# Kernel tuning notes

Measured on AMD Instinct MI355X. Metric: run time of the kernel, lower is better.

The kernel has to match this reference:

```python
import jax, jax.numpy as jnp
import numpy as np


def setup_inputs() -> dict:
    key = jax.random.key(0)
    k1, k2, k3, k4 = jax.random.split(key, 4)
    bs, n, f_in, f_out, n_head = 8, 2048, 64, 32, 4
    return {
        "h": jax.random.normal(k1, (bs, n, f_in), dtype=jnp.float32),
        "w": jax.random.normal(k2, (n_head, f_in, f_out), dtype=jnp.float32) * 0.1,
        "a_src": jax.random.normal(k3, (n_head, f_out, 1), dtype=jnp.float32) * 0.1,
        "a_dst": jax.random.normal(k4, (n_head, f_out, 1), dtype=jnp.float32) * 0.1,
        "b": jnp.zeros((f_out,), dtype=jnp.float32),
    }


def reference(h, w, a_src, a_dst, b):
    # h: [bs, n, f_in], w: [H, f_in, f_out]
    # h_prime: [bs, H, n, f_out]
    h_prime = jnp.einsum("bnf,hfo->bhno", h, w)
    # additive scores: attn_src[b,h,i] + attn_dst[b,h,j]
    attn_src = jnp.einsum("bhno,ho->bhn", h_prime, a_src[..., 0])  # [bs,H,n]
    attn_dst = jnp.einsum("bhno,ho->bhn", h_prime, a_dst[..., 0])  # [bs,H,n]
    attn = attn_src[:, :, :, None] + attn_dst[:, :, None, :]       # [bs,H,n,n]
    attn = jax.nn.leaky_relu(attn, negative_slope=0.2)
    attn = jax.nn.softmax(attn, axis=-1)
    # dropout with p=0.0 (eval) is identity
    output = jnp.einsum("bhij,bhjo->bhio", attn, h_prime) + b
    return (output, attn)
```

## Files before the change

### kernel.cpp

```cpp
#include <hip/hip_runtime.h>
#include <hip/hip_bf16.h>

#define BS 8
#define NH 4
#define NSEQ 2048
#define FIN 64
#define FOUT 32
#define CH 32
#define BHH (BS*NH)
#define NBINS 8192
#define LOG2E 1.44269504088896340736f

typedef float f32x4 __attribute__((ext_vector_type(4)));

#define WSS_SE    0
#define WSS_DE    (WSS_SE + BHH*NSEQ)
#define WSS_INVL  (WSS_DE + BHH*NSEQ)
#define WSS_KEY   (WSS_INVL + BHH*NSEQ)
#define WSS_SUFL  (WSS_KEY + BHH*NSEQ)
#define WSS_PREL  (WSS_SUFL + BHH*NSEQ)
#define WSS_TOTP  (WSS_PREL + BHH*NSEQ)
#define WSS_TOTN  (WSS_TOTP + BHH*16)
#define WSS_VTOTP (WSS_TOTN + BHH*16)
#define WSS_VTOTN (WSS_VTOTP + BHH*16*CH)
#define WSS_FTOT  (WSS_VTOTN + BHH*16*CH)
#define WSI_SIDX  0

#define BIG_HP    0
#define BIG_SUFP  (BIG_HP + BHH*NSEQ*CH)
#define BIG_PREN  (BIG_SUFP + BHH*NSEQ*CH)
#define BIG_TOTAL (BIG_PREN + BHH*NSEQ*CH)

__global__ __launch_bounds__(256) void k1_proj(
    const float* __restrict__ h, const float* __restrict__ w,
    const float* __restrict__ asrc, const float* __restrict__ adst,
    float* __restrict__ ws, float* __restrict__ big)
{
    __shared__ float hl[64*65];
    const int b  = blockIdx.x >> 5;
    const int i0 = (blockIdx.x & 31) * 64;
    const int tid = threadIdx.x;
    const float* hsrc = h + ((size_t)b*NSEQ + i0)*FIN;
    for (int x = tid; x < 64*64; x += 256) hl[(x>>6)*65 + (x&63)] = hsrc[x];
    __syncthreads();
    const int head = __builtin_amdgcn_readfirstlane(tid >> 6);
    const int r = tid & 63;
    const int i = i0 + r;
    float acc[FOUT];
#pragma unroll
    for (int o=0;o<FOUT;o++) acc[o]=0.f;
    const float* wh = w + head*FIN*FOUT;
    for (int f=0; f<FIN; f++) {
        const float hv = hl[r*65+f];
#pragma unroll
        for (int o=0;o<FOUT;o++) acc[o] += hv * wh[f*FOUT+o];
    }
    const float* as = asrc + head*FOUT;
    const float* ad = adst + head*FOUT;
    float s=0.f, d=0.f;
#pragma unroll
    for (int o=0;o<FOUT;o++){ s += acc[o]*as[o]; d += acc[o]*ad[o]; }
    const int bh = b*NH + head;
    float* hp = big + BIG_HP + ((size_t)bh*NSEQ + i)*CH;
#pragma unroll
    for (int o=0;o<FOUT;o+=4) { f32x4 v = {acc[o],acc[o+1],acc[o+2],acc[o+3]}; *(f32x4*)(hp+o)=v; }
    ws[WSS_SE + bh*NSEQ + i] = s * LOG2E;
    ws[WSS_DE + bh*NSEQ + i] = d * LOG2E;
}

__global__ __launch_bounds__(1024) void kh_sort(
    float* __restrict__ ws, int* __restrict__ wsi)
{
    __shared__ int hist[NBINS];
    __shared__ int wtot[16];
    const int bh = blockIdx.x;
    const int tid = threadIdx.x;
    const int wv = tid >> 6, lane = tid & 63;
    const float x0 = ws[WSS_DE + bh*NSEQ + tid];
    const float x1 = ws[WSS_DE + bh*NSEQ + tid + 1024];
    for (int bb=tid; bb<NBINS; bb+=1024) hist[bb]=0;
    __syncthreads();
    int b0 = (int)((x0 + 8.0f)*512.0f); b0 = b0 > NBINS-1 ? NBINS-1 : (b0 < 0 ? 0 : b0);
    int b1 = (int)((x1 + 8.0f)*512.0f); b1 = b1 > NBINS-1 ? NBINS-1 : (b1 < 0 ? 0 : b1);
    atomicAdd(&hist[b0],1); atomicAdd(&hist[b1],1);
    __syncthreads();
    int loc[8]; int tsum=0;
#pragma unroll
    for (int k=0;k<8;k++){ loc[k]=tsum; tsum += hist[tid*8+k]; }
    int inc = tsum;
#pragma unroll
    for (int off=1; off<64; off<<=1){ int v=__shfl_up(inc,off); if (lane>=off) inc+=v; }
    if (lane==63) wtot[wv]=inc;
    const int laneex = inc - tsum;
    __syncthreads();
    if (tid==0){ int a=0; for (int k=0;k<16;k++){ int v=wtot[k]; wtot[k]=a; a+=v; } }
    __syncthreads();
    const int base = wtot[wv] + laneex;
#pragma unroll
    for (int k=0;k<8;k++) hist[tid*8+k] = base + loc[k];
    __syncthreads();
    {
        int p0 = atomicAdd(&hist[b0],1);
        ws[WSS_KEY + bh*NSEQ + p0] = x0; wsi[WSI_SIDX + bh*NSEQ + p0] = tid;
        int p1 = atomicAdd(&hist[b1],1);
        ws[WSS_KEY + bh*NSEQ + p1] = x1; wsi[WSI_SIDX + bh*NSEQ + p1] = tid + 1024;
    }
}

__global__ __launch_bounds__(256) void k2b(
    float* __restrict__ ws, const int* __restrict__ wsi, float* __restrict__ big)
{
    __shared__ float kk[128];
    __shared__ int   si[128];
    __shared__ float SP[128][CH];
    __shared__ float SN[128][CH];
    const int bid = blockIdx.x;
    const int bh = bid >> 4, c = bid & 15;
    const int tid = threadIdx.x, wv = tid>>6, lane = tid&63;
    if (tid < 128) {
        kk[tid] = ws[WSS_KEY + bh*NSEQ + c*128 + tid];
        si[tid] = wsi[WSI_SIDX + bh*NSEQ + c*128 + tid];
    }
    __syncthreads();
    const float* hpb = big + BIG_HP + (size_t)bh*NSEQ*CH;
    const int half = lane >> 5, ch = lane & 31;
#pragma unroll 4
    for (int t=0; t<16; t++) {
        const int rr = wv*32 + t*2 + half;
        const float dk = kk[rr];
        const float v  = hpb[(size_t)si[rr]*CH + ch];
        SP[rr][ch] = __builtin_amdgcn_exp2f(dk)      * v;
        SN[rr][ch] = __builtin_amdgcn_exp2f(0.2f*dk) * v;
    }
    __syncthreads();
    const size_t tb = (size_t)bh*NSEQ + c*128;
    if (wv == 0 && lane < CH) {
        float acc = 0.f;
        for (int rr=127; rr>=0; rr--) {
            acc += SP[rr][lane];
            big[BIG_SUFP + (tb + rr)*CH + lane] = acc;
        }
        ws[WSS_VTOTP + (bh*16 + c)*CH + lane] = acc;
    } else if (wv == 1 && lane < CH) {
        float acc = 0.f;
        for (int rr=0; rr<128; rr++) {
            big[BIG_PREN + (tb + rr)*CH + lane] = acc;
            acc += SN[rr][lane];
        }
        ws[WSS_VTOTN + (bh*16 + c)*CH + lane] = acc;
    } else if (wv == 2 && lane == 0) {
        float acc = 0.f;
        for (int rr=127; rr>=0; rr--) {
            acc += __builtin_amdgcn_exp2f(kk[rr]);
            ws[WSS_SUFL + tb + rr] = acc;
        }
        ws[WSS_TOTP + bh*16 + c] = acc;
    } else if (wv == 3 && lane == 0) {
        float acc = 0.f;
        for (int rr=0; rr<128; rr++) {
            ws[WSS_PREL + tb + rr] = acc;
            acc += __builtin_amdgcn_exp2f(0.2f*kk[rr]);
        }
        ws[WSS_TOTN + bh*16 + c] = acc;
    }
}

__global__ __launch_bounds__(256) void k2c(
    float* __restrict__ ws, const float* __restrict__ big,
    const float* __restrict__ bvec, float* __restrict__ outp)
{
    __shared__ float keys[NSEQ];
    __shared__ float sufl[NSEQ];
    __shared__ float prel[NSEQ];
    __shared__ float vofP[17][CH];
    __shared__ float vofN[17][CH];
    __shared__ float sofP[17], sofN[17];
    __shared__ int   krow[128];
    __shared__ float invrow[128], e1row[128], e2row[128];
    const int bid = blockIdx.x;
    const int bh = bid >> 4, q = bid & 15;
    const int tid = threadIdx.x, wv = tid>>6, lane = tid&63;
    for (int x = tid; x < NSEQ; x += 256) {
        keys[x] = ws[WSS_KEY  + bh*NSEQ + x];
        sufl[x] = ws[WSS_SUFL + bh*NSEQ + x];
        prel[x] = ws[WSS_PREL + bh*NSEQ + x];
    }
    if (tid < CH) {
        float a = 0.f;
        for (int c=15; c>=0; c--) { vofP[c][tid] = a; a += ws[WSS_VTOTP + (bh*16+c)*CH + tid]; }
        vofP[16][tid] = 0.f;
        a = 0.f;
        for (int c=0; c<16; c++) { vofN[c][tid] = a; a += ws[WSS_VTOTN + (bh*16+c)*CH + tid]; }
        vofN[16][tid] = a;
    } else if (tid == 64) {
        float a = 0.f;
        for (int c=15; c>=0; c--) { sofP[c] = a; a += ws[WSS_TOTP + bh*16 + c]; }
        sofP[16] = 0.f;
        a = 0.f;
        for (int c=0; c<16; c++) { sofN[c] = a; a += ws[WSS_TOTN + bh*16 + c]; }
        sofN[16] = a;
    }
    __syncthreads();
    if (tid < 128) {
        const int i = q*128 + tid;
        const float sp = ws[WSS_SE + bh*NSEQ + i];
        const float tau = -sp;
        int lo=0, hi=NSEQ;
        while (lo < hi) { const int mid=(lo+hi)>>1; if (keys[mid] < tau) lo=mid+1; else hi=mid; }
        const float e1 = __builtin_amdgcn_exp2f(sp);
        const float e2 = __builtin_amdgcn_exp2f(0.2f*sp);
        const float Ss = (lo==NSEQ) ? 0.f        : sufl[lo] + sofP[lo>>7];
        const float Ns = (lo==NSEQ) ? sofN[16]   : prel[lo] + sofN[lo>>7];
        const float inv = 1.0f / (e1*Ss + e2*Ns);
        ws[WSS_INVL + bh*NSEQ + i] = inv;
        krow[tid]=lo; invrow[tid]=inv; e1row[tid]=e1; e2row[tid]=e2;
    }
    __syncthreads();
    const int half = lane >> 5, ch = lane & 31;
    const float bval = bvec[ch];
    const size_t tb = (size_t)bh*NSEQ;
#pragma unroll 4
    for (int t=0; t<16; t++) {
        const int r = wv*32 + t*2 + half;
        const int k = krow[r];
        const float S = (k==NSEQ) ? 0.f      : big[BIG_SUFP + (tb + k)*CH + ch] + vofP[k>>7][ch];
        const float N = (k==NSEQ) ? vofN[16][ch] : big[BIG_PREN + (tb + k)*CH + ch] + vofN[k>>7][ch];
        outp[(tb + q*128 + r)*CH + ch] = (e1row[r]*S + e2row[r]*N)*invrow[r] + bval;
    }
}

__global__ __launch_bounds__(256) void k3b_attn(
    const float* __restrict__ ws, float* __restrict__ attn)
{
    __shared__ float E1[NSEQ];
    __shared__ float E2[NSEQ];
    __shared__ float rA[32], rB[32], rT[32];
    const int bid = blockIdx.x;
    const int swz = (bid & 7) * 256 + (bid >> 3);
    const int bh = swz >> 6;
    const int i0 = (swz & 63) * 32;
    const int tid = threadIdx.x;
    for (int x = tid; x < NSEQ; x += 256) {
        const float d = ws[WSS_DE + bh*NSEQ + x];
        E1[x] = __builtin_amdgcn_exp2f(d);
        E2[x] = __builtin_amdgcn_exp2f(0.2f*d);
    }
    if (tid < 32) {
        const float sp  = ws[WSS_SE   + bh*NSEQ + i0 + tid];
        const float inv = ws[WSS_INVL + bh*NSEQ + i0 + tid];
        rA[tid] = __builtin_amdgcn_exp2f(sp)      * inv;
        rB[tid] = __builtin_amdgcn_exp2f(0.2f*sp) * inv;
        rT[tid] = __builtin_amdgcn_exp2f(-sp);
    }
    __syncthreads();
    const int wv = tid>>6, lane = tid&63;
    float A[8], B[8], T[8];
#pragma unroll
    for (int k=0;k<8;k++){ A[k]=rA[wv*8+k]; B[k]=rB[wv*8+k]; T[k]=rT[wv*8+k]; }
    float* rbase = attn + ((size_t)bh*NSEQ + i0 + wv*8)*NSEQ;
#pragma unroll
    for (int blk=0; blk<8; blk++) {
        const int j0 = blk*256 + lane*4;
        const f32x4 e1 = *(const f32x4*)&E1[j0];
        const f32x4 e2 = *(const f32x4*)&E2[j0];
#pragma unroll
        for (int k=0;k<8;k++) {
            f32x4 p;
            p.x = (e1.x >= T[k]) ? A[k]*e1.x : B[k]*e2.x;
            p.y = (e1.y >= T[k]) ? A[k]*e1.y : B[k]*e2.y;
            p.z = (e1.z >= T[k]) ? A[k]*e1.z : B[k]*e2.z;
            p.w = (e1.w >= T[k]) ? A[k]*e1.w : B[k]*e2.w;
            *(f32x4*)(rbase + (size_t)k*NSEQ + j0) = p;
        }
    }
}

extern "C" void kernel_launch(void* const* d_in, const int* in_sizes, int n_in,
                              void* d_out, int out_size, void* d_ws, size_t ws_size,
                              hipStream_t stream)
{
    (void)in_sizes; (void)n_in; (void)out_size; (void)ws_size;
    const float* h    = (const float*)d_in[0];
    const float* w    = (const float*)d_in[1];
    const float* asrc = (const float*)d_in[2];
    const float* adst = (const float*)d_in[3];
    const float* bvec = (const float*)d_in[4];
    float* outp = (float*)d_out;
    float* attn = outp + (size_t)BHH*NSEQ*FOUT;
    float* big  = attn + (size_t)BHH*NSEQ*NSEQ - BIG_TOTAL;
    float* ws   = (float*)d_ws;
    int*   wsi  = (int*)(ws + WSS_FTOT);

    k1_proj  <<<BS*32,   256, 0, stream>>>(h, w, asrc, adst, ws, big);
    kh_sort  <<<BHH,    1024, 0, stream>>>(ws, wsi);
    k2b      <<<BHH*16,  256, 0, stream>>>(ws, wsi, big);
    k2c      <<<BHH*16,  256, 0, stream>>>(ws, big, bvec, outp);
    k3b_attn <<<BHH*64,  256, 0, stream>>>(ws, attn);
}
```

Measured before the change: 158.8 us.

## Fuse output and attention-write kernels when workspace can hold scratch buffers

Adds a combined kernel that, per 32-row tile, computes the softmax normaliser by binary search, writes the output rows and then writes the attention rows. This removes one launch and the round trip of the inverse-normaliser array. To do this the large scratch buffers move from the tail of the attn output into the workspace, since the fused kernel overwrites attn while still reading them. The fused path only runs if the workspace is large enough; otherwise the old two-kernel path is kept. The cost is that every 32-row block now reloads keys, prefix sums and offsets, which adds shared-memory traffic and larger LDS use per block.

```diff
diff --git a/kernel.cpp b/kernel.cpp
--- a/kernel.cpp
+++ b/kernel.cpp
@@ -25,6 +25,7 @@
 #define WSS_VTOTN (WSS_VTOTP + BHH*16*CH)
 #define WSS_FTOT  (WSS_VTOTN + BHH*16*CH)
 #define WSI_SIDX  0
+#define WSI_ITOT  (WSI_SIDX + BHH*NSEQ)
 
 #define BIG_HP    0
 #define BIG_SUFP  (BIG_HP + BHH*NSEQ*CH)
@@ -165,22 +166,28 @@
     }
 }
 
-__global__ __launch_bounds__(256) void k2c(
-    float* __restrict__ ws, const float* __restrict__ big,
-    const float* __restrict__ bvec, float* __restrict__ outp)
-{
-    __shared__ float keys[NSEQ];
-    __shared__ float sufl[NSEQ];
-    __shared__ float prel[NSEQ];
-    __shared__ float vofP[17][CH];
-    __shared__ float vofN[17][CH];
+__global__ __launch_bounds__(256) void k3mega(
+    const float* __restrict__ ws, const float* __restrict__ big,
+    const float* __restrict__ bvec, float* __restrict__ outp,
+    float* __restrict__ attn)
+{
+    __shared__ float E1[NSEQ], E2[NSEQ];
+    __shared__ float keys[NSEQ], sufl[NSEQ], prel[NSEQ];
+    __shared__ float vofP[17][CH], vofN[17][CH];
     __shared__ float sofP[17], sofN[17];
-    __shared__ int   krow[128];
-    __shared__ float invrow[128], e1row[128], e2row[128];
+    __shared__ int   krow[32];
+    __shared__ float e1r[32], e2r[32], invr[32], Tr[32];
     const int bid = blockIdx.x;
-    const int bh = bid >> 4, q = bid & 15;
-    const int tid = threadIdx.x, wv = tid>>6, lane = tid&63;
+    const int swz = (bid & 7) * 256 + (bid >> 3);
+    const int bh = swz >> 6;
+    const int i0 = (swz & 63) * 32;
+    const int tid = threadIdx.x;
+    const int wv = tid>>6, lane = tid&63;
+
     for (int x = tid; x < NSEQ; x += 256) {
+        const float d = ws[WSS_DE + bh*NSEQ + x];
+        E1[x] = __builtin_amdgcn_exp2f(d);
+        E2[x] = __builtin_amdgcn_exp2f(0.2f*d);
         keys[x] = ws[WSS_KEY  + bh*NSEQ + x];
         sufl[x] = ws[WSS_SUFL + bh*NSEQ + x];
         prel[x] = ws[WSS_PREL + bh*NSEQ + x];
@@ -201,6 +208,94 @@
         sofN[16] = a;
     }
     __syncthreads();
+
+    if (tid < 32) {
+        const int i = i0 + tid;
+        const float sp = ws[WSS_SE + bh*NSEQ + i];
+        const float tau = -sp;
+        int lo=0, hi=NSEQ;
+        while (lo < hi) { const int mid=(lo+hi)>>1; if (keys[mid] < tau) lo=mid+1; else hi=mid; }
+        const float e1 = __builtin_amdgcn_exp2f(sp);
+        const float e2 = __builtin_amdgcn_exp2f(0.2f*sp);
+        const float Ss = (lo==NSEQ) ? 0.f      : sufl[lo] + sofP[lo>>7];
+        const float Ns = (lo==NSEQ) ? sofN[16] : prel[lo] + sofN[lo>>7];
+        const float inv = 1.0f / (e1*Ss + e2*Ns);
+        krow[tid]=lo; e1r[tid]=e1; e2r[tid]=e2; invr[tid]=inv;
+        Tr[tid] = __builtin_amdgcn_exp2f(-sp);
+    }
+    __syncthreads();
+
+    {
+        const int half = lane >> 5, ch = lane & 31;
+        const float bval = bvec[ch];
+        const size_t tb = (size_t)bh*NSEQ;
+#pragma unroll
+        for (int t=0; t<4; t++) {
+            const int r = wv*8 + t*2 + half;
+            const int k = krow[r];
+            const float S = (k==NSEQ) ? 0.f          : big[BIG_SUFP + (tb + k)*CH + ch] + vofP[k>>7][ch];
+            const float N = (k==NSEQ) ? vofN[16][ch] : big[BIG_PREN + (tb + k)*CH + ch] + vofN[k>>7][ch];
+            outp[(tb + i0 + r)*CH + ch] = (e1r[r]*S + e2r[r]*N)*invr[r] + bval;
+        }
+    }
+
+    float A[8], B[8], T[8];
+#pragma unroll
+    for (int k=0;k<8;k++){
+        const int r = wv*8+k;
+        A[k]=e1r[r]*invr[r]; B[k]=e2r[r]*invr[r]; T[k]=Tr[r];
+    }
+    float* rbase = attn + ((size_t)bh*NSEQ + i0 + wv*8)*NSEQ;
+#pragma unroll
+    for (int blk=0; blk<8; blk++) {
+        const int j0 = blk*256 + lane*4;
+        const f32x4 e1 = *(const f32x4*)&E1[j0];
+        const f32x4 e2 = *(const f32x4*)&E2[j0];
+#pragma unroll
+        for (int k=0;k<8;k++) {
+            f32x4 p;
+            p.x = (e1.x >= T[k]) ? A[k]*e1.x : B[k]*e2.x;
+            p.y = (e1.y >= T[k]) ? A[k]*e1.y : B[k]*e2.y;
+            p.z = (e1.z >= T[k]) ? A[k]*e1.z : B[k]*e2.z;
+            p.w = (e1.w >= T[k]) ? A[k]*e1.w : B[k]*e2.w;
+            *(f32x4*)(rbase + (size_t)k*NSEQ + j0) = p;
+        }
+    }
+}
+
+__global__ __launch_bounds__(256) void k2c(
+    float* __restrict__ ws, const float* __restrict__ big,
+    const float* __restrict__ bvec, float* __restrict__ outp)
+{
+    __shared__ float keys[NSEQ], sufl[NSEQ], prel[NSEQ];
+    __shared__ float vofP[17][CH], vofN[17][CH];
+    __shared__ float sofP[17], sofN[17];
+    __shared__ int   krow[128];
+    __shared__ float invrow[128], e1row[128], e2row[128];
+    const int bid = blockIdx.x;
+    const int bh = bid >> 4, q = bid & 15;
+    const int tid = threadIdx.x, wv = tid>>6, lane = tid&63;
+    for (int x = tid; x < NSEQ; x += 256) {
+        keys[x] = ws[WSS_KEY  + bh*NSEQ + x];
+        sufl[x] = ws[WSS_SUFL + bh*NSEQ + x];
+        prel[x] = ws[WSS_PREL + bh*NSEQ + x];
+    }
+    if (tid < CH) {
+        float a = 0.f;
+        for (int c=15; c>=0; c--) { vofP[c][tid] = a; a += ws[WSS_VTOTP + (bh*16+c)*CH + tid]; }
+        vofP[16][tid] = 0.f;
+        a = 0.f;
+        for (int c=0; c<16; c++) { vofN[c][tid] = a; a += ws[WSS_VTOTN + (bh*16+c)*CH + tid]; }
+        vofN[16][tid] = a;
+    } else if (tid == 64) {
+        float a = 0.f;
+        for (int c=15; c>=0; c--) { sofP[c] = a; a += ws[WSS_TOTP + bh*16 + c]; }
+        sofP[16] = 0.f;
+        a = 0.f;
+        for (int c=0; c<16; c++) { sofN[c] = a; a += ws[WSS_TOTN + bh*16 + c]; }
+        sofN[16] = a;
+    }
+    __syncthreads();
     if (tid < 128) {
         const int i = q*128 + tid;
         const float sp = ws[WSS_SE + bh*NSEQ + i];
@@ -209,8 +304,8 @@
         while (lo < hi) { const int mid=(lo+hi)>>1; if (keys[mid] < tau) lo=mid+1; else hi=mid; }
         const float e1 = __builtin_amdgcn_exp2f(sp);
         const float e2 = __builtin_amdgcn_exp2f(0.2f*sp);
-        const float Ss = (lo==NSEQ) ? 0.f        : sufl[lo] + sofP[lo>>7];
-        const float Ns = (lo==NSEQ) ? sofN[16]   : prel[lo] + sofN[lo>>7];
+        const float Ss = (lo==NSEQ) ? 0.f      : sufl[lo] + sofP[lo>>7];
+        const float Ns = (lo==NSEQ) ? sofN[16] : prel[lo] + sofN[lo>>7];
         const float inv = 1.0f / (e1*Ss + e2*Ns);
         ws[WSS_INVL + bh*NSEQ + i] = inv;
         krow[tid]=lo; invrow[tid]=inv; e1row[tid]=e1; e2row[tid]=e2;
@@ -223,7 +318,7 @@
     for (int t=0; t<16; t++) {
         const int r = wv*32 + t*2 + half;
         const int k = krow[r];
-        const float S = (k==NSEQ) ? 0.f      : big[BIG_SUFP + (tb + k)*CH + ch] + vofP[k>>7][ch];
+        const float S = (k==NSEQ) ? 0.f          : big[BIG_SUFP + (tb + k)*CH + ch] + vofP[k>>7][ch];
         const float N = (k==NSEQ) ? vofN[16][ch] : big[BIG_PREN + (tb + k)*CH + ch] + vofN[k>>7][ch];
         outp[(tb + q*128 + r)*CH + ch] = (e1row[r]*S + e2row[r]*N)*invrow[r] + bval;
     }
@@ -232,8 +327,7 @@
 __global__ __launch_bounds__(256) void k3b_attn(
     const float* __restrict__ ws, float* __restrict__ attn)
 {
-    __shared__ float E1[NSEQ];
-    __shared__ float E2[NSEQ];
+    __shared__ float E1[NSEQ], E2[NSEQ];
     __shared__ float rA[32], rB[32], rT[32];
     const int bid = blockIdx.x;
     const int swz = (bid & 7) * 256 + (bid >> 3);
@@ -279,7 +373,7 @@
                               void* d_out, int out_size, void* d_ws, size_t ws_size,
                               hipStream_t stream)
 {
-    (void)in_sizes; (void)n_in; (void)out_size; (void)ws_size;
+    (void)in_sizes; (void)n_in; (void)out_size;
     const float* h    = (const float*)d_in[0];
     const float* w    = (const float*)d_in[1];
     const float* asrc = (const float*)d_in[2];
@@ -287,13 +381,21 @@
     const float* bvec = (const float*)d_in[4];
     float* outp = (float*)d_out;
     float* attn = outp + (size_t)BHH*NSEQ*FOUT;
-    float* big  = attn + (size_t)BHH*NSEQ*NSEQ - BIG_TOTAL;
     float* ws   = (float*)d_ws;
     int*   wsi  = (int*)(ws + WSS_FTOT);
+
+    const size_t need_bytes = ((size_t)WSS_FTOT + WSI_ITOT + BIG_TOTAL) * 4 + 1024;
+    const bool bigInWs = (ws_size >= need_bytes);
+    float* big = bigInWs ? (float*)(wsi + WSI_ITOT)
+                         : attn + (size_t)BHH*NSEQ*NSEQ - BIG_TOTAL;
 
     k1_proj  <<<BS*32,   256, 0, stream>>>(h, w, asrc, adst, ws, big);
     kh_sort  <<<BHH,    1024, 0, stream>>>(ws, wsi);
     k2b      <<<BHH*16,  256, 0, stream>>>(ws, wsi, big);
-    k2c      <<<BHH*16,  256, 0, stream>>>(ws, big, bvec, outp);
-    k3b_attn <<<BHH*64,  256, 0, stream>>>(ws, attn);
-}
+    if (bigInWs) {
+        k3mega <<<BHH*64, 256, 0, stream>>>(ws, big, bvec, outp, attn);
+    } else {
+        k2c      <<<BHH*16, 256, 0, stream>>>(ws, big, bvec, outp);
+        k3b_attn <<<BHH*64, 256, 0, stream>>>(ws, attn);
+    }
+}
```

New measurement: 159.9 us. Within noise of the previous version (+0.7%).

## Precompute exp tables in sort kernel, use fmax for softmax branch, halve histogram bins

Applied to the files above, without the earlier changes.

The sort kernel now computes exp2(d) and exp2(0.2d) once per column and stores them in workspace, so the attention-writing kernel loads them instead of recomputing them in all 64 row blocks per head. The per-element leaky-relu branch compare against a threshold is replaced by fmaxf of the two scaled exponentials, which is equivalent because both paths share the same row normaliser. This drops the rT table and the compare. The histogram shrinks to 4096 bins, halving scan work and LDS use. Scratch buffers move from the tail of the attn output into the workspace when it is large enough, which avoids a write-then-overwrite dependency on output memory but requires a larger workspace.

```diff
diff --git a/kernel.cpp b/kernel.cpp
--- a/kernel.cpp
+++ b/kernel.cpp
@@ -8,7 +8,7 @@
 #define FOUT 32
 #define CH 32
 #define BHH (BS*NH)
-#define NBINS 8192
+#define NBINS 4096
 #define LOG2E 1.44269504088896340736f
 
 typedef float f32x4 __attribute__((ext_vector_type(4)));
@@ -17,7 +17,9 @@
 #define WSS_DE    (WSS_SE + BHH*NSEQ)
 #define WSS_INVL  (WSS_DE + BHH*NSEQ)
 #define WSS_KEY   (WSS_INVL + BHH*NSEQ)
-#define WSS_SUFL  (WSS_KEY + BHH*NSEQ)
+#define WSS_E1T   (WSS_KEY + BHH*NSEQ)
+#define WSS_E2T   (WSS_E1T + BHH*NSEQ)
+#define WSS_SUFL  (WSS_E2T + BHH*NSEQ)
 #define WSS_PREL  (WSS_SUFL + BHH*NSEQ)
 #define WSS_TOTP  (WSS_PREL + BHH*NSEQ)
 #define WSS_TOTN  (WSS_TOTP + BHH*16)
@@ -25,6 +27,7 @@
 #define WSS_VTOTN (WSS_VTOTP + BHH*16*CH)
 #define WSS_FTOT  (WSS_VTOTN + BHH*16*CH)
 #define WSI_SIDX  0
+#define WSI_ITOT  (WSI_SIDX + BHH*NSEQ)
 
 #define BIG_HP    0
 #define BIG_SUFP  (BIG_HP + BHH*NSEQ*CH)
@@ -78,15 +81,19 @@
     const int wv = tid >> 6, lane = tid & 63;
     const float x0 = ws[WSS_DE + bh*NSEQ + tid];
     const float x1 = ws[WSS_DE + bh*NSEQ + tid + 1024];
+    ws[WSS_E1T + bh*NSEQ + tid]        = __builtin_amdgcn_exp2f(x0);
+    ws[WSS_E2T + bh*NSEQ + tid]        = __builtin_amdgcn_exp2f(0.2f*x0);
+    ws[WSS_E1T + bh*NSEQ + tid + 1024] = __builtin_amdgcn_exp2f(x1);
+    ws[WSS_E2T + bh*NSEQ + tid + 1024] = __builtin_amdgcn_exp2f(0.2f*x1);
     for (int bb=tid; bb<NBINS; bb+=1024) hist[bb]=0;
     __syncthreads();
-    int b0 = (int)((x0 + 8.0f)*512.0f); b0 = b0 > NBINS-1 ? NBINS-1 : (b0 < 0 ? 0 : b0);
-    int b1 = (int)((x1 + 8.0f)*512.0f); b1 = b1 > NBINS-1 ? NBINS-1 : (b1 < 0 ? 0 : b1);
+    int b0 = (int)((x0 + 8.0f)*256.0f); b0 = b0 > NBINS-1 ? NBINS-1 : (b0 < 0 ? 0 : b0);
+    int b1 = (int)((x1 + 8.0f)*256.0f); b1 = b1 > NBINS-1 ? NBINS-1 : (b1 < 0 ? 0 : b1);
     atomicAdd(&hist[b0],1); atomicAdd(&hist[b1],1);
     __syncthreads();
-    int loc[8]; int tsum=0;
-#pragma unroll
-    for (int k=0;k<8;k++){ loc[k]=tsum; tsum += hist[tid*8+k]; }
+    int loc[4]; int tsum=0;
+#pragma unroll
+    for (int k=0;k<4;k++){ loc[k]=tsum; tsum += hist[tid*4+k]; }
     int inc = tsum;
 #pragma unroll
     for (int off=1; off<64; off<<=1){ int v=__shfl_up(inc,off); if (lane>=off) inc+=v; }
@@ -97,7 +104,7 @@
     __syncthreads();
     const int base = wtot[wv] + laneex;
 #pragma unroll
-    for (int k=0;k<8;k++) hist[tid*8+k] = base + loc[k];
+    for (int k=0;k<4;k++) hist[tid*4+k] = base + loc[k];
     __syncthreads();
     {
         int p0 = atomicAdd(&hist[b0],1);
@@ -169,11 +176,8 @@
     float* __restrict__ ws, const float* __restrict__ big,
     const float* __restrict__ bvec, float* __restrict__ outp)
 {
-    __shared__ float keys[NSEQ];
-    __shared__ float sufl[NSEQ];
-    __shared__ float prel[NSEQ];
-    __shared__ float vofP[17][CH];
-    __shared__ float vofN[17][CH];
+    __shared__ float keys[NSEQ], sufl[NSEQ], prel[NSEQ];
+    __shared__ float vofP[17][CH], vofN[17][CH];
     __shared__ float sofP[17], sofN[17];
     __shared__ int   krow[128];
     __shared__ float invrow[128], e1row[128], e2row[128];
@@ -209,8 +213,8 @@
         while (lo < hi) { const int mid=(lo+hi)>>1; if (keys[mid] < tau) lo=mid+1; else hi=mid; }
         const float e1 = __builtin_amdgcn_exp2f(sp);
         const float e2 = __builtin_amdgcn_exp2f(0.2f*sp);
-        const float Ss = (lo==NSEQ) ? 0.f        : sufl[lo] + sofP[lo>>7];
-        const float Ns = (lo==NSEQ) ? sofN[16]   : prel[lo] + sofN[lo>>7];
+        const float Ss = (lo==NSEQ) ? 0.f      : sufl[lo] + sofP[lo>>7];
+        const float Ns = (lo==NSEQ) ? sofN[16] : prel[lo] + sofN[lo>>7];
         const float inv = 1.0f / (e1*Ss + e2*Ns);
         ws[WSS_INVL + bh*NSEQ + i] = inv;
         krow[tid]=lo; invrow[tid]=inv; e1row[tid]=e1; e2row[tid]=e2;
@@ -223,7 +227,7 @@
     for (int t=0; t<16; t++) {
         const int r = wv*32 + t*2 + half;
         const int k = krow[r];
-        const float S = (k==NSEQ) ? 0.f      : big[BIG_SUFP + (tb + k)*CH + ch] + vofP[k>>7][ch];
+        const float S = (k==NSEQ) ? 0.f          : big[BIG_SUFP + (tb + k)*CH + ch] + vofP[k>>7][ch];
         const float N = (k==NSEQ) ? vofN[16][ch] : big[BIG_PREN + (tb + k)*CH + ch] + vofN[k>>7][ch];
         outp[(tb + q*128 + r)*CH + ch] = (e1row[r]*S + e2row[r]*N)*invrow[r] + bval;
     }
@@ -232,31 +236,28 @@
 __global__ __launch_bounds__(256) void k3b_attn(
     const float* __restrict__ ws, float* __restrict__ attn)
 {
-    __shared__ float E1[NSEQ];
-    __shared__ float E2[NSEQ];
-    __shared__ float rA[32], rB[32], rT[32];
+    __shared__ float E1[NSEQ], E2[NSEQ];
+    __shared__ float rA[32], rB[32];
     const int bid = blockIdx.x;
     const int swz = (bid & 7) * 256 + (bid >> 3);
     const int bh = swz >> 6;
     const int i0 = (swz & 63) * 32;
     const int tid = threadIdx.x;
     for (int x = tid; x < NSEQ; x += 256) {
-        const float d = ws[WSS_DE + bh*NSEQ + x];
-        E1[x] = __builtin_amdgcn_exp2f(d);
-        E2[x] = __builtin_amdgcn_exp2f(0.2f*d);
+        E1[x] = ws[WSS_E1T + bh*NSEQ + x];
+        E2[x] = ws[WSS_E2T + bh*NSEQ + x];
     }
     if (tid < 32) {
         const float sp  = ws[WSS_SE   + bh*NSEQ + i0 + tid];
         const float inv = ws[WSS_INVL + bh*NSEQ + i0 + tid];
         rA[tid] = __builtin_amdgcn_exp2f(sp)      * inv;
         rB[tid] = __builtin_amdgcn_exp2f(0.2f*sp) * inv;
-        rT[tid] = __builtin_amdgcn_exp2f(-sp);
     }
     __syncthreads();
     const int wv = tid>>6, lane = tid&63;
-    float A[8], B[8], T[8];
-#pragma unroll
-    for (int k=0;k<8;k++){ A[k]=rA[wv*8+k]; B[k]=rB[wv*8+k]; T[k]=rT[wv*8+k]; }
+    float A[8], B[8];
+#pragma unroll
+    for (int k=0;k<8;k++){ A[k]=rA[wv*8+k]; B[k]=rB[wv*8+k]; }
     float* rbase = attn + ((size_t)bh*NSEQ + i0 + wv*8)*NSEQ;
 #pragma unroll
     for (int blk=0; blk<8; blk++) {
@@ -266,10 +267,10 @@
 #pragma unroll
         for (int k=0;k<8;k++) {
             f32x4 p;
-            p.x = (e1.x >= T[k]) ? A[k]*e1.x : B[k]*e2.x;
-            p.y = (e1.y >= T[k]) ? A[k]*e1.y : B[k]*e2.y;
-            p.z = (e1.z >= T[k]) ? A[k]*e1.z : B[k]*e2.z;
-            p.w = (e1.w >= T[k]) ? A[k]*e1.w : B[k]*e2.w;
+            p.x = fmaxf(A[k]*e1.x, B[k]*e2.x);
+            p.y = fmaxf(A[k]*e1.y, B[k]*e2.y);
+            p.z = fmaxf(A[k]*e1.z, B[k]*e2.z);
+            p.w = fmaxf(A[k]*e1.w, B[k]*e2.w);
             *(f32x4*)(rbase + (size_t)k*NSEQ + j0) = p;
         }
     }
@@ -279,7 +280,7 @@
                               void* d_out, int out_size, void* d_ws, size_t ws_size,
                               hipStream_t stream)
 {
-    (void)in_sizes; (void)n_in; (void)out_size; (void)ws_size;
+    (void)in_sizes; (void)n_in; (void)out_size;
     const float* h    = (const float*)d_in[0];
     const float* w    = (const float*)d_in[1];
     const float* asrc = (const float*)d_in[2];
@@ -287,9 +288,12 @@
     const float* bvec = (const float*)d_in[4];
     float* outp = (float*)d_out;
     float* attn = outp + (size_t)BHH*NSEQ*FOUT;
-    float* big  = attn + (size_t)BHH*NSEQ*NSEQ - BIG_TOTAL;
     float* ws   = (float*)d_ws;
     int*   wsi  = (int*)(ws + WSS_FTOT);
+
+    const size_t need_bytes = ((size_t)WSS_FTOT + WSI_ITOT + BIG_TOTAL) * 4 + 1024;
+    float* big = (ws_size >= need_bytes) ? (float*)(wsi + WSI_ITOT)
+                                         : attn + (size_t)BHH*NSEQ*NSEQ - BIG_TOTAL;
 
     k1_proj  <<<BS*32,   256, 0, stream>>>(h, w, asrc, adst, ws, big);
     kh_sort  <<<BHH,    1024, 0, stream>>>(ws, wsi);
```

Result: slower. 162.9 us (+2.6%).
